# Kernel tuning notes

Measured on AMD Instinct MI355X. Metric: run time of the kernel, lower is better.

## Reference

```python
import jax, jax.numpy as jnp
import numpy as np

N_NODES = 100000
N_EDGES = 1600000
D_FEAT = 128
HIDDEN = 128
N_CLASSES = 10
NUM_GRAPHS = 64


def setup_inputs() -> dict:
    key = jax.random.key(0)
    ks = jax.random.split(key, 12)
    x = jax.random.normal(ks[0], (N_NODES, D_FEAT), dtype=jnp.float32)
    edge_index = jax.random.randint(ks[1], (2, N_EDGES), 0, N_NODES, dtype=jnp.int32)
    batch = jnp.sort(jax.random.randint(ks[2], (N_NODES,), 0, NUM_GRAPHS, dtype=jnp.int32))
    s = 1.0 / np.sqrt(HIDDEN)
    def lin(k, out_d, in_d):
        return jax.random.uniform(k, (out_d, in_d), jnp.float32, -s, s)
    return {
        "x": x,
        "edge_index": edge_index,
        "batch": batch,
        "W1l": lin(ks[3], HIDDEN, D_FEAT), "b1": jnp.zeros((HIDDEN,), jnp.float32),
        "W1r": lin(ks[4], HIDDEN, D_FEAT),
        "W2l": lin(ks[5], HIDDEN, HIDDEN), "b2": jnp.zeros((HIDDEN,), jnp.float32),
        "W2r": lin(ks[6], HIDDEN, HIDDEN),
        "W3l": lin(ks[7], HIDDEN, HIDDEN), "b3": jnp.zeros((HIDDEN,), jnp.float32),
        "W3r": lin(ks[8], HIDDEN, HIDDEN),
        "Wout": lin(ks[9], N_CLASSES, HIDDEN), "bout": jnp.zeros((N_CLASSES,), jnp.float32),
    }


def reference(x, edge_index, batch, W1l, b1, W1r, W2l, b2, W2r, W3l, b3, W3r, Wout, bout):
    src, dst = edge_index[0], edge_index[1]
    n = x.shape[0]

    def sage(h, Wl, b, Wr):
        # sum-aggregate neighbor features: scatter-add x[src] into dst rows
        agg = jax.ops.segment_sum(h[src], dst, num_segments=n)  # [N, d]
        return agg @ Wl.T + b + h @ Wr.T

    h = jax.nn.relu(sage(x, W1l, b1, W1r))
    h = jax.nn.relu(sage(h, W2l, b2, W2r))
    h = sage(h, W3l, b3, W3r)
    pooled = jax.ops.segment_sum(h, batch, num_segments=NUM_GRAPHS)  # [G, hidden]
    # dropout is identity in eval mode
    return pooled @ Wout.T + bout
```

## Files before the change

### kernel.cpp

```cpp
#include <hip/hip_runtime.h>
#include <hip/hip_bf16.h>

#define N_NODES  100000
#define N_EDGES  1600000
#define D_FEAT   128
#define HIDDEN   128
#define N_CLASSES 10
#define NUM_GRAPHS 64

#define NBUCK 250
#define NPB   400
#define BCAP  7168
#define GT    64
#define NPAD  100096
#define NTILES (NPAD / GT)

typedef __bf16 bf16x8 __attribute__((ext_vector_type(8)));
typedef float  f32x4  __attribute__((ext_vector_type(4)));

static __device__ __forceinline__ unsigned short f2bf(float f) {
    __bf16 b = (__bf16)f;
    return __builtin_bit_cast(unsigned short, b);
}

static __device__ __forceinline__ void async_copy16(void* lds, const void* g) {
    __builtin_amdgcn_global_load_lds(
        (const __attribute__((address_space(1))) void*)g,
        (__attribute__((address_space(3))) void*)lds, 16, 0, 0);
}

__global__ void conv_w6_kernel(const float* __restrict__ W0, const float* __restrict__ W1,
                               const float* __restrict__ W2, const float* __restrict__ W3,
                               const float* __restrict__ W4, const float* __restrict__ W5,
                               __bf16* __restrict__ out) {
    const float* Ws[6] = {W0, W1, W2, W3, W4, W5};
    int m = blockIdx.x >> 6;
    int i = (blockIdx.x & 63) * 256 + threadIdx.x;
    out[m * (HIDDEN * D_FEAT) + i] = (__bf16)Ws[m][i];
}

__global__ __launch_bounds__(256) void xconv_kernel(const float* __restrict__ x,
                                                    __bf16* __restrict__ out) {
    int i = blockIdx.x * 256 + threadIdx.x;
    bf16x8 o;
    if (i < N_NODES * 128 / 8) {
        float4 v0 = ((const float4*)x)[i * 2];
        float4 v1 = ((const float4*)x)[i * 2 + 1];
        o[0] = (__bf16)v0.x; o[1] = (__bf16)v0.y; o[2] = (__bf16)v0.z; o[3] = (__bf16)v0.w;
        o[4] = (__bf16)v1.x; o[5] = (__bf16)v1.y; o[6] = (__bf16)v1.z; o[7] = (__bf16)v1.w;
    } else {
        #pragma unroll
        for (int k = 0; k < 8; k++) o[k] = (__bf16)0.f;
    }
    if (i < NPAD * 128 / 8) ((bf16x8*)out)[i] = o;
}

__global__ __launch_bounds__(256) void bucket_scatter_kernel(const int* __restrict__ ei,
                                                             int* __restrict__ gcur,
                                                             int2* __restrict__ bkt) {
    __shared__ int h[NBUCK];
    __shared__ int lb[NBUCK];
    int t = threadIdx.x;
    const int CH = N_EDGES / 256;
    for (int i = t; i < NBUCK; i += 256) h[i] = 0;
    __syncthreads();
    int e0 = blockIdx.x * CH;
    for (int e = e0 + t; e < e0 + CH; e += 256) {
        int d = ei[N_EDGES + e];
        atomicAdd(&h[d / NPB], 1);
    }
    __syncthreads();
    for (int i = t; i < NBUCK; i += 256) {
        lb[i] = atomicAdd(&gcur[i], h[i]);
        h[i] = 0;
    }
    __syncthreads();
    for (int e = e0 + t; e < e0 + CH; e += 256) {
        int s = ei[e];
        int d = ei[N_EDGES + e];
        int bb = d / NPB;
        int pos = lb[bb] + atomicAdd(&h[bb], 1);
        if (pos < BCAP) bkt[(size_t)bb * BCAP + pos] = make_int2(s, d);
    }
}

__global__ __launch_bounds__(256) void bucket_csr_kernel(const int2* __restrict__ bkt,
                                                         const int* __restrict__ gcur,
                                                         int2* __restrict__ rpse,
                                                         int* __restrict__ csr_src) {
    const int b = blockIdx.x;
    const int n0 = b * NPB;
    const int base = b * BCAP;
    int m = gcur[b]; if (m > BCAP) m = BCAP;
    __shared__ int cnt[NPB];
    __shared__ int part[128];
    __shared__ int excl[NPB];
    int t = threadIdx.x;
    for (int i = t; i < NPB; i += 256) cnt[i] = 0;
    __syncthreads();
    for (int e = t; e < m; e += 256) {
        int2 p = bkt[base + e];
        atomicAdd(&cnt[p.y - n0], 1);
    }
    __syncthreads();
    int gs = 0;
    if (t < 100) { gs = cnt[4 * t] + cnt[4 * t + 1] + cnt[4 * t + 2] + cnt[4 * t + 3]; part[t] = gs; }
    else if (t < 128) part[t] = 0;
    __syncthreads();
    for (int off = 1; off < 128; off <<= 1) {
        int x = 0;
        if (t < 128 && t >= off) x = part[t - off];
        __syncthreads();
        if (t < 128) part[t] += x;
        __syncthreads();
    }
    if (t < 100) part[t] -= gs;
    __syncthreads();
    for (int i = t; i < NPB; i += 256) {
        int g = i >> 2;
        int e0 = part[g];
        for (int j = g * 4; j < i; j++) e0 += cnt[j];
        excl[i] = e0;
    }
    __syncthreads();
    for (int i = t; i < NPB; i += 256) {
        rpse[n0 + i] = make_int2(base + excl[i], base + excl[i] + cnt[i]);
    }
    __syncthreads();
    for (int i = t; i < NPB; i += 256) cnt[i] = excl[i];
    __syncthreads();
    for (int e = t; e < m; e += 256) {
        int2 p = bkt[base + e];
        int pos = base + atomicAdd(&cnt[p.y - n0], 1);
        csr_src[pos] = p.x;
    }
}

__global__ __launch_bounds__(256) void gather_kernel(
    const __bf16* __restrict__ h, const int2* __restrict__ rpse,
    const int* __restrict__ csr_src, __bf16* __restrict__ agg, int N)
{
    int nid = blockIdx.x * 16 + (threadIdx.x >> 4);
    if (nid >= N) return;
    int f8 = threadIdx.x & 15;
    int2 se = rpse[nid];

    float a[8] = {0.f, 0.f, 0.f, 0.f, 0.f, 0.f, 0.f, 0.f};

    int j = se.x;
    for (; j + 3 < se.y; j += 4) {
        int s0 = csr_src[j];
        int s1 = csr_src[j + 1];
        int s2 = csr_src[j + 2];
        int s3 = csr_src[j + 3];
        bf16x8 u0 = ((const bf16x8*)h)[(size_t)s0 * 16 + f8];
        bf16x8 u1 = ((const bf16x8*)h)[(size_t)s1 * 16 + f8];
        bf16x8 u2 = ((const bf16x8*)h)[(size_t)s2 * 16 + f8];
        bf16x8 u3 = ((const bf16x8*)h)[(size_t)s3 * 16 + f8];
        #pragma unroll
        for (int i = 0; i < 8; i++)
            a[i] += ((float)u0[i] + (float)u1[i]) + ((float)u2[i] + (float)u3[i]);
    }
    for (; j < se.y; j++) {
        int s0 = csr_src[j];
        bf16x8 u0 = ((const bf16x8*)h)[(size_t)s0 * 16 + f8];
        #pragma unroll
        for (int i = 0; i < 8; i++) a[i] += (float)u0[i];
    }
    bf16x8 o;
    #pragma unroll
    for (int i = 0; i < 8; i++) o[i] = (__bf16)a[i];
    ((bf16x8*)agg)[(size_t)nid * 16 + f8] = o;
}

template<bool RELU>
__global__ __launch_bounds__(256) void fused_gemm_kernel(
    const __bf16* __restrict__ hA,
    const __bf16* __restrict__ hG,
    const __bf16* __restrict__ Wl, const __bf16* __restrict__ Wr,
    const float* __restrict__ bias,
    __bf16* __restrict__ outp, int M)
{
    __shared__ __bf16 lds[2][GT * 128];

    const int tid  = threadIdx.x;
    const int wave = tid >> 6;
    const int lane = tid & 63;
    const int kq = lane >> 4;
    const int ln = lane & 15;
    const int node_base = blockIdx.x * GT;
    const int f_base = wave * 32;

    {
        const __bf16* gsrc = hG + (size_t)node_base * 128;
        const __bf16* asrc = hA + (size_t)node_base * 128;
        #pragma unroll
        for (int i = 0; i < 4; i++) {
            int u = i * 256 + tid;
            int row = u >> 4;
            int sc = (u & 15) ^ (row & 15);
            async_copy16(&lds[0][u * 8], gsrc + row * 128 + sc * 8);
            async_copy16(&lds[1][u * 8], asrc + row * 128 + sc * 8);
        }
    }

    bf16x8 wfragL[2][4], wfragR[2][4];
    #pragma unroll
    for (int t = 0; t < 2; t++) {
        int wrow = f_base + t * 16 + ln;
        #pragma unroll
        for (int kc = 0; kc < 4; kc++) {
            int k0 = kc * 32 + kq * 8;
            wfragL[t][kc] = *(const bf16x8*)(Wl + wrow * 128 + k0);
            wfragR[t][kc] = *(const bf16x8*)(Wr + wrow * 128 + k0);
        }
    }
    float4 bias4[2];
    bias4[0] = *(const float4*)(bias + f_base + kq * 4);
    bias4[1] = *(const float4*)(bias + f_base + 16 + kq * 4);

    __syncthreads();

    #pragma unroll 2
    for (int tau = 0; tau < GT / 16; tau++) {
        int r = tau * 16 + ln;
        bf16x8 gfrag[4], afrag[4];
        #pragma unroll
        for (int kc = 0; kc < 4; kc++) {
            int c = (4 * kc + kq) ^ ln;
            gfrag[kc] = *(const bf16x8*)&lds[0][r * 128 + c * 8];
            afrag[kc] = *(const bf16x8*)&lds[1][r * 128 + c * 8];
        }

        f32x4 acc[2] = {(f32x4)(0.f), (f32x4)(0.f)};
        #pragma unroll
        for (int kc = 0; kc < 4; kc++) {
            #pragma unroll
            for (int t = 0; t < 2; t++) {
                acc[t] = __builtin_amdgcn_mfma_f32_16x16x32_bf16(wfragL[t][kc], gfrag[kc], acc[t], 0, 0, 0);
                acc[t] = __builtin_amdgcn_mfma_f32_16x16x32_bf16(wfragR[t][kc], afrag[kc], acc[t], 0, 0, 0);
            }
        }

        int node = node_base + tau * 16 + ln;
        if (node < M) {
            size_t rowoff = (size_t)node * 128;
            #pragma unroll
            for (int t = 0; t < 2; t++) {
                int fc = f_base + t * 16 + kq * 4;
                ushort4 o;
                float v0 = acc[t][0] + bias4[t].x;
                float v1 = acc[t][1] + bias4[t].y;
                float v2 = acc[t][2] + bias4[t].z;
                float v3 = acc[t][3] + bias4[t].w;
                if (RELU) {
                    v0 = fmaxf(v0, 0.f); v1 = fmaxf(v1, 0.f);
                    v2 = fmaxf(v2, 0.f); v3 = fmaxf(v3, 0.f);
                }
                o.x = f2bf(v0); o.y = f2bf(v1); o.z = f2bf(v2); o.w = f2bf(v3);
                *(ushort4*)(outp + rowoff + fc) = o;
            }
        }
    }
}

__global__ __launch_bounds__(256) void pool_kernel(
    const __bf16* __restrict__ h, const int* __restrict__ batch,
    float* __restrict__ pooled, int N)
{
    int idx = blockIdx.x * 256 + threadIdx.x;
    int f = idx & 127;
    int chunk = idx >> 7;
    int n0 = chunk * 32;
    if (n0 >= N) return;
    int n1 = n0 + 32; if (n1 > N) n1 = N;
    int curb = batch[n0];
    float acc = 0.f;
    for (int n = n0; n < n1; n++) {
        int b = batch[n];
        if (b != curb) {
            unsafeAtomicAdd(&pooled[(size_t)curb * 128 + f], acc);
            acc = 0.f; curb = b;
        }
        acc += (float)h[(size_t)n * 128 + f];
    }
    unsafeAtomicAdd(&pooled[(size_t)curb * 128 + f], acc);
}

__global__ void final_gemm_kernel(
    const float* __restrict__ pooled, const float* __restrict__ Wout,
    const float* __restrict__ bout, float* __restrict__ out)
{
    int idx = blockIdx.x * 64 + threadIdx.x;
    if (idx < NUM_GRAPHS * N_CLASSES) {
        int g = idx / N_CLASSES;
        int c = idx % N_CLASSES;
        float acc = bout[c];
        for (int k = 0; k < HIDDEN; k++)
            acc += pooled[g * HIDDEN + k] * Wout[c * HIDDEN + k];
        out[idx] = acc;
    }
}

extern "C" void kernel_launch(void* const* d_in, const int* in_sizes, int n_in,
                              void* d_out, int out_size, void* d_ws, size_t ws_size,
                              hipStream_t stream) {
    const float* x     = (const float*)d_in[0];
    const int*   ei    = (const int*)d_in[1];
    const int*   batch = (const int*)d_in[2];
    const float* W1l = (const float*)d_in[3];
    const float* b1  = (const float*)d_in[4];
    const float* W1r = (const float*)d_in[5];
    const float* W2l = (const float*)d_in[6];
    const float* b2  = (const float*)d_in[7];
    const float* W2r = (const float*)d_in[8];
    const float* W3l = (const float*)d_in[9];
    const float* b3  = (const float*)d_in[10];
    const float* W3r = (const float*)d_in[11];
    const float* Wout = (const float*)d_in[12];
    const float* bout = (const float*)d_in[13];
    float* out = (float*)d_out;

    char* ws = (char*)d_ws;
    size_t off = 0;
    const size_t NB = (size_t)NPAD * 128 * sizeof(__bf16);
    __bf16* B0    = (__bf16*)(ws + off); off += NB;
    __bf16* B1    = (__bf16*)(ws + off); off += NB;
    __bf16* B2    = (__bf16*)(ws + off); off += NB;
    float* pooled = (float*)(ws + off);  off += (size_t)NUM_GRAPHS * HIDDEN * sizeof(float);
    __bf16* wbf   = (__bf16*)(ws + off); off += 6 * (size_t)HIDDEN * D_FEAT * sizeof(__bf16);
    int2* rpse    = (int2*)(ws + off);   off += (size_t)N_NODES * sizeof(int2);
    int* csr_src  = (int*)(ws + off);    off += (size_t)NBUCK * BCAP * sizeof(int);
    int2* bkt     = (int2*)(ws + off);   off += (size_t)NBUCK * BCAP * sizeof(int2);
    int* gcur     = (int*)(ws + off);    off += (NBUCK + 8) * sizeof(int);

    const int WSZ = HIDDEN * D_FEAT;

    conv_w6_kernel<<<6 * 64, 256, 0, stream>>>(W1l, W1r, W2l, W2r, W3l, W3r, wbf);
    xconv_kernel<<<NPAD * 128 / (256 * 8), 256, 0, stream>>>(x, B0);

    hipMemsetAsync(gcur, 0, NBUCK * sizeof(int), stream);
    bucket_scatter_kernel<<<256, 256, 0, stream>>>(ei, gcur, bkt);
    bucket_csr_kernel<<<NBUCK, 256, 0, stream>>>(bkt, gcur, rpse, csr_src);

    const int gath_grid = (N_NODES + 15) / 16;

    gather_kernel<<<gath_grid, 256, 0, stream>>>(B0, rpse, csr_src, B1, N_NODES);
    fused_gemm_kernel<true><<<NTILES, 256, 0, stream>>>(B0, B1, wbf + 0 * WSZ, wbf + 1 * WSZ, b1, B2, N_NODES);

    gather_kernel<<<gath_grid, 256, 0, stream>>>(B2, rpse, csr_src, B1, N_NODES);
    fused_gemm_kernel<true><<<NTILES, 256, 0, stream>>>(B2, B1, wbf + 2 * WSZ, wbf + 3 * WSZ, b2, B0, N_NODES);

    gather_kernel<<<gath_grid, 256, 0, stream>>>(B0, rpse, csr_src, B1, N_NODES);
    fused_gemm_kernel<false><<<NTILES, 256, 0, stream>>>(B0, B1, wbf + 4 * WSZ, wbf + 5 * WSZ, b3, B2, N_NODES);

    hipMemsetAsync(pooled, 0, (size_t)NUM_GRAPHS * HIDDEN * sizeof(float), stream);
    const int pool_grid = ((N_NODES + 31) / 32 * 128 + 255) / 256;
    pool_kernel<<<pool_grid, 256, 0, stream>>>(B2, batch, pooled, N_NODES);
    final_gemm_kernel<<<10, 64, 0, stream>>>(pooled, Wout, bout, out);
}
```

Before: 433.5 us.

## Fuse neighbor gather, dual GEMM, and pooling into one per-layer kernel

Merges the gather kernel and the fused GEMM into a single per-layer kernel. Each 16-node block aggregates neighbor features into LDS and then runs MFMA on them, so the intermediate aggregate buffer never goes to global memory. The last layer pools directly through shuffle-reduced atomics instead of writing h and running a separate pool kernel. Bucket entries are also packed into one 32-bit int instead of an int2, which halves the sort traffic. In exchange, the tiles are small, so every block reloads all weight fragments, and the final layer issues many more atomics.

```diff
diff --git a/kernel.cpp b/kernel.cpp
--- a/kernel.cpp
+++ b/kernel.cpp
@@ -11,9 +11,8 @@
 #define NBUCK 250
 #define NPB   400
 #define BCAP  7168
-#define GT    64
-#define NPAD  100096
-#define NTILES (NPAD / GT)
+#define TN    16
+#define NBLK  (N_NODES / TN)
 
 typedef __bf16 bf16x8 __attribute__((ext_vector_type(8)));
 typedef float  f32x4  __attribute__((ext_vector_type(4)));
@@ -21,12 +20,6 @@
 static __device__ __forceinline__ unsigned short f2bf(float f) {
     __bf16 b = (__bf16)f;
     return __builtin_bit_cast(unsigned short, b);
-}
-
-static __device__ __forceinline__ void async_copy16(void* lds, const void* g) {
-    __builtin_amdgcn_global_load_lds(
-        (const __attribute__((address_space(1))) void*)g,
-        (__attribute__((address_space(3))) void*)lds, 16, 0, 0);
 }
 
 __global__ void conv_w6_kernel(const float* __restrict__ W0, const float* __restrict__ W1,
@@ -42,22 +35,17 @@
 __global__ __launch_bounds__(256) void xconv_kernel(const float* __restrict__ x,
                                                     __bf16* __restrict__ out) {
     int i = blockIdx.x * 256 + threadIdx.x;
+    float4 v0 = ((const float4*)x)[i * 2];
+    float4 v1 = ((const float4*)x)[i * 2 + 1];
     bf16x8 o;
-    if (i < N_NODES * 128 / 8) {
-        float4 v0 = ((const float4*)x)[i * 2];
-        float4 v1 = ((const float4*)x)[i * 2 + 1];
-        o[0] = (__bf16)v0.x; o[1] = (__bf16)v0.y; o[2] = (__bf16)v0.z; o[3] = (__bf16)v0.w;
-        o[4] = (__bf16)v1.x; o[5] = (__bf16)v1.y; o[6] = (__bf16)v1.z; o[7] = (__bf16)v1.w;
-    } else {
-        #pragma unroll
-        for (int k = 0; k < 8; k++) o[k] = (__bf16)0.f;
-    }
-    if (i < NPAD * 128 / 8) ((bf16x8*)out)[i] = o;
+    o[0] = (__bf16)v0.x; o[1] = (__bf16)v0.y; o[2] = (__bf16)v0.z; o[3] = (__bf16)v0.w;
+    o[4] = (__bf16)v1.x; o[5] = (__bf16)v1.y; o[6] = (__bf16)v1.z; o[7] = (__bf16)v1.w;
+    ((bf16x8*)out)[i] = o;
 }
 
 __global__ __launch_bounds__(256) void bucket_scatter_kernel(const int* __restrict__ ei,
                                                              int* __restrict__ gcur,
-                                                             int2* __restrict__ bkt) {
+                                                             int* __restrict__ bkt) {
     __shared__ int h[NBUCK];
     __shared__ int lb[NBUCK];
     int t = threadIdx.x;
@@ -80,11 +68,11 @@
         int d = ei[N_EDGES + e];
         int bb = d / NPB;
         int pos = lb[bb] + atomicAdd(&h[bb], 1);
-        if (pos < BCAP) bkt[(size_t)bb * BCAP + pos] = make_int2(s, d);
-    }
-}
-
-__global__ __launch_bounds__(256) void bucket_csr_kernel(const int2* __restrict__ bkt,
+        if (pos < BCAP) bkt[(size_t)bb * BCAP + pos] = ((d - bb * NPB) << 17) | s;
+    }
+}
+
+__global__ __launch_bounds__(256) void bucket_csr_kernel(const int* __restrict__ bkt,
                                                          const int* __restrict__ gcur,
                                                          int2* __restrict__ rpse,
                                                          int* __restrict__ csr_src) {
@@ -99,8 +87,8 @@
     for (int i = t; i < NPB; i += 256) cnt[i] = 0;
     __syncthreads();
     for (int e = t; e < m; e += 256) {
-        int2 p = bkt[base + e];
-        atomicAdd(&cnt[p.y - n0], 1);
+        int p = bkt[base + e];
+        atomicAdd(&cnt[p >> 17], 1);
     }
     __syncthreads();
     int gs = 0;
@@ -130,79 +118,65 @@
     for (int i = t; i < NPB; i += 256) cnt[i] = excl[i];
     __syncthreads();
     for (int e = t; e < m; e += 256) {
-        int2 p = bkt[base + e];
-        int pos = base + atomicAdd(&cnt[p.y - n0], 1);
-        csr_src[pos] = p.x;
-    }
-}
-
-__global__ __launch_bounds__(256) void gather_kernel(
-    const __bf16* __restrict__ h, const int2* __restrict__ rpse,
-    const int* __restrict__ csr_src, __bf16* __restrict__ agg, int N)
-{
-    int nid = blockIdx.x * 16 + (threadIdx.x >> 4);
-    if (nid >= N) return;
-    int f8 = threadIdx.x & 15;
-    int2 se = rpse[nid];
-
-    float a[8] = {0.f, 0.f, 0.f, 0.f, 0.f, 0.f, 0.f, 0.f};
-
-    int j = se.x;
-    for (; j + 3 < se.y; j += 4) {
-        int s0 = csr_src[j];
-        int s1 = csr_src[j + 1];
-        int s2 = csr_src[j + 2];
-        int s3 = csr_src[j + 3];
-        bf16x8 u0 = ((const bf16x8*)h)[(size_t)s0 * 16 + f8];
-        bf16x8 u1 = ((const bf16x8*)h)[(size_t)s1 * 16 + f8];
-        bf16x8 u2 = ((const bf16x8*)h)[(size_t)s2 * 16 + f8];
-        bf16x8 u3 = ((const bf16x8*)h)[(size_t)s3 * 16 + f8];
-        #pragma unroll
-        for (int i = 0; i < 8; i++)
-            a[i] += ((float)u0[i] + (float)u1[i]) + ((float)u2[i] + (float)u3[i]);
-    }
-    for (; j < se.y; j++) {
-        int s0 = csr_src[j];
-        bf16x8 u0 = ((const bf16x8*)h)[(size_t)s0 * 16 + f8];
-        #pragma unroll
-        for (int i = 0; i < 8; i++) a[i] += (float)u0[i];
-    }
-    bf16x8 o;
-    #pragma unroll
-    for (int i = 0; i < 8; i++) o[i] = (__bf16)a[i];
-    ((bf16x8*)agg)[(size_t)nid * 16 + f8] = o;
-}
-
-template<bool RELU>
-__global__ __launch_bounds__(256) void fused_gemm_kernel(
-    const __bf16* __restrict__ hA,
-    const __bf16* __restrict__ hG,
+        int p = bkt[base + e];
+        int pos = base + atomicAdd(&cnt[p >> 17], 1);
+        csr_src[pos] = p & 0x1FFFF;
+    }
+}
+
+template<bool RELU, bool POOL>
+__global__ __launch_bounds__(256, 3) void fused_layer_kernel(
+    const __bf16* __restrict__ h,
+    const int2* __restrict__ rpse,
+    const int* __restrict__ csr_src,
     const __bf16* __restrict__ Wl, const __bf16* __restrict__ Wr,
     const float* __restrict__ bias,
-    __bf16* __restrict__ outp, int M)
+    __bf16* __restrict__ outp,
+    const int* __restrict__ batch,
+    float* __restrict__ pooled)
 {
-    __shared__ __bf16 lds[2][GT * 128];
-
-    const int tid  = threadIdx.x;
+    __shared__ __bf16 ldsT[TN * 128];
+
+    const int tid = threadIdx.x;
+    const int grp = tid >> 4;
+    const int f8  = tid & 15;
+    const int nid_base = blockIdx.x * TN;
+
+    {
+        const int node_g = nid_base + grp;
+        int2 se = rpse[node_g];
+        float a[8] = {0.f, 0.f, 0.f, 0.f, 0.f, 0.f, 0.f, 0.f};
+        int j = se.x;
+        for (; j + 3 < se.y; j += 4) {
+            int s0 = csr_src[j];
+            int s1 = csr_src[j + 1];
+            int s2 = csr_src[j + 2];
+            int s3 = csr_src[j + 3];
+            bf16x8 u0 = ((const bf16x8*)h)[(size_t)s0 * 16 + f8];
+            bf16x8 u1 = ((const bf16x8*)h)[(size_t)s1 * 16 + f8];
+            bf16x8 u2 = ((const bf16x8*)h)[(size_t)s2 * 16 + f8];
+            bf16x8 u3 = ((const bf16x8*)h)[(size_t)s3 * 16 + f8];
+            #pragma unroll
+            for (int i = 0; i < 8; i++)
+                a[i] += ((float)u0[i] + (float)u1[i]) + ((float)u2[i] + (float)u3[i]);
+        }
+        for (; j < se.y; j++) {
+            int s0 = csr_src[j];
+            bf16x8 u0 = ((const bf16x8*)h)[(size_t)s0 * 16 + f8];
+            #pragma unroll
+            for (int i = 0; i < 8; i++) a[i] += (float)u0[i];
+        }
+        bf16x8 o;
+        #pragma unroll
+        for (int i = 0; i < 8; i++) o[i] = (__bf16)a[i];
+        ((bf16x8*)ldsT)[grp * 16 + (f8 ^ grp)] = o;
+    }
+
     const int wave = tid >> 6;
     const int lane = tid & 63;
     const int kq = lane >> 4;
     const int ln = lane & 15;
-    const int node_base = blockIdx.x * GT;
     const int f_base = wave * 32;
-
-    {
-        const __bf16* gsrc = hG + (size_t)node_base * 128;
-        const __bf16* asrc = hA + (size_t)node_base * 128;
-        #pragma unroll
-        for (int i = 0; i < 4; i++) {
-            int u = i * 256 + tid;
-            int row = u >> 4;
-            int sc = (u & 15) ^ (row & 15);
-            async_copy16(&lds[0][u * 8], gsrc + row * 128 + sc * 8);
-            async_copy16(&lds[1][u * 8], asrc + row * 128 + sc * 8);
-        }
-    }
 
     bf16x8 wfragL[2][4], wfragR[2][4];
     #pragma unroll
@@ -219,72 +193,84 @@
     bias4[0] = *(const float4*)(bias + f_base + kq * 4);
     bias4[1] = *(const float4*)(bias + f_base + 16 + kq * 4);
 
-    __syncthreads();
-
-    #pragma unroll 2
-    for (int tau = 0; tau < GT / 16; tau++) {
-        int r = tau * 16 + ln;
-        bf16x8 gfrag[4], afrag[4];
-        #pragma unroll
-        for (int kc = 0; kc < 4; kc++) {
-            int c = (4 * kc + kq) ^ ln;
-            gfrag[kc] = *(const bf16x8*)&lds[0][r * 128 + c * 8];
-            afrag[kc] = *(const bf16x8*)&lds[1][r * 128 + c * 8];
-        }
-
-        f32x4 acc[2] = {(f32x4)(0.f), (f32x4)(0.f)};
-        #pragma unroll
-        for (int kc = 0; kc < 4; kc++) {
-            #pragma unroll
-            for (int t = 0; t < 2; t++) {
-                acc[t] = __builtin_amdgcn_mfma_f32_16x16x32_bf16(wfragL[t][kc], gfrag[kc], acc[t], 0, 0, 0);
-                acc[t] = __builtin_amdgcn_mfma_f32_16x16x32_bf16(wfragR[t][kc], afrag[kc], acc[t], 0, 0, 0);
+    const int node_s = nid_base + ln;
+    bf16x8 afrag[4];
+    #pragma unroll
+    for (int kc = 0; kc < 4; kc++)
+        afrag[kc] = *(const bf16x8*)(h + (size_t)node_s * 128 + kc * 32 + kq * 8);
+
+    __syncthreads();
+
+    bf16x8 gfrag[4];
+    #pragma unroll
+    for (int kc = 0; kc < 4; kc++)
+        gfrag[kc] = ((const bf16x8*)ldsT)[ln * 16 + ((4 * kc + kq) ^ ln)];
+
+    f32x4 acc[2] = {(f32x4)(0.f), (f32x4)(0.f)};
+    #pragma unroll
+    for (int kc = 0; kc < 4; kc++) {
+        #pragma unroll
+        for (int t = 0; t < 2; t++) {
+            acc[t] = __builtin_amdgcn_mfma_f32_16x16x32_bf16(wfragL[t][kc], gfrag[kc], acc[t], 0, 0, 0);
+            acc[t] = __builtin_amdgcn_mfma_f32_16x16x32_bf16(wfragR[t][kc], afrag[kc], acc[t], 0, 0, 0);
+        }
+    }
+
+    if (!POOL) {
+        size_t rowoff = (size_t)node_s * 128;
+        #pragma unroll
+        for (int t = 0; t < 2; t++) {
+            int fc = f_base + t * 16 + kq * 4;
+            float v0 = acc[t][0] + bias4[t].x;
+            float v1 = acc[t][1] + bias4[t].y;
+            float v2 = acc[t][2] + bias4[t].z;
+            float v3 = acc[t][3] + bias4[t].w;
+            if (RELU) {
+                v0 = fmaxf(v0, 0.f); v1 = fmaxf(v1, 0.f);
+                v2 = fmaxf(v2, 0.f); v3 = fmaxf(v3, 0.f);
             }
-        }
-
-        int node = node_base + tau * 16 + ln;
-        if (node < M) {
-            size_t rowoff = (size_t)node * 128;
-            #pragma unroll
-            for (int t = 0; t < 2; t++) {
-                int fc = f_base + t * 16 + kq * 4;
-                ushort4 o;
-                float v0 = acc[t][0] + bias4[t].x;
-                float v1 = acc[t][1] + bias4[t].y;
-                float v2 = acc[t][2] + bias4[t].z;
-                float v3 = acc[t][3] + bias4[t].w;
-                if (RELU) {
-                    v0 = fmaxf(v0, 0.f); v1 = fmaxf(v1, 0.f);
-                    v2 = fmaxf(v2, 0.f); v3 = fmaxf(v3, 0.f);
+            ushort4 o;
+            o.x = f2bf(v0); o.y = f2bf(v1); o.z = f2bf(v2); o.w = f2bf(v3);
+            *(ushort4*)(outp + rowoff + fc) = o;
+        }
+    } else {
+        const int b = batch[node_s];
+        const bool uni = (batch[nid_base] == batch[nid_base + TN - 1]);
+        #pragma unroll
+        for (int t = 0; t < 2; t++) {
+            int fc = f_base + t * 16 + kq * 4;
+            float v0 = acc[t][0] + bias4[t].x;
+            float v1 = acc[t][1] + bias4[t].y;
+            float v2 = acc[t][2] + bias4[t].z;
+            float v3 = acc[t][3] + bias4[t].w;
+            if (RELU) {
+                v0 = fmaxf(v0, 0.f); v1 = fmaxf(v1, 0.f);
+                v2 = fmaxf(v2, 0.f); v3 = fmaxf(v3, 0.f);
+            }
+            if (uni) {
+                #pragma unroll
+                for (int m = 1; m < 16; m <<= 1) {
+                    v0 += __shfl_xor(v0, m);
+                    v1 += __shfl_xor(v1, m);
+                    v2 += __shfl_xor(v2, m);
+                    v3 += __shfl_xor(v3, m);
                 }
-                o.x = f2bf(v0); o.y = f2bf(v1); o.z = f2bf(v2); o.w = f2bf(v3);
-                *(ushort4*)(outp + rowoff + fc) = o;
+                if (ln == 0) {
+                    float* p = &pooled[(size_t)b * HIDDEN + fc];
+                    unsafeAtomicAdd(p + 0, v0);
+                    unsafeAtomicAdd(p + 1, v1);
+                    unsafeAtomicAdd(p + 2, v2);
+                    unsafeAtomicAdd(p + 3, v3);
+                }
+            } else {
+                float* p = &pooled[(size_t)b * HIDDEN + fc];
+                unsafeAtomicAdd(p + 0, v0);
+                unsafeAtomicAdd(p + 1, v1);
+                unsafeAtomicAdd(p + 2, v2);
+                unsafeAtomicAdd(p + 3, v3);
             }
         }
     }
-}
-
-__global__ __launch_bounds__(256) void pool_kernel(
-    const __bf16* __restrict__ h, const int* __restrict__ batch,
-    float* __restrict__ pooled, int N)
-{
-    int idx = blockIdx.x * 256 + threadIdx.x;
-    int f = idx & 127;
-    int chunk = idx >> 7;
-    int n0 = chunk * 32;
-    if (n0 >= N) return;
-    int n1 = n0 + 32; if (n1 > N) n1 = N;
-    int curb = batch[n0];
-    float acc = 0.f;
-    for (int n = n0; n < n1; n++) {
-        int b = batch[n];
-        if (b != curb) {
-            unsafeAtomicAdd(&pooled[(size_t)curb * 128 + f], acc);
-            acc = 0.f; curb = b;
-        }
-        acc += (float)h[(size_t)n * 128 + f];
-    }
-    unsafeAtomicAdd(&pooled[(size_t)curb * 128 + f], acc);
 }
 
 __global__ void final_gemm_kernel(
@@ -323,39 +309,32 @@
 
     char* ws = (char*)d_ws;
     size_t off = 0;
-    const size_t NB = (size_t)NPAD * 128 * sizeof(__bf16);
+    const size_t NB = (size_t)N_NODES * 128 * sizeof(__bf16);
     __bf16* B0    = (__bf16*)(ws + off); off += NB;
-    __bf16* B1    = (__bf16*)(ws + off); off += NB;
     __bf16* B2    = (__bf16*)(ws + off); off += NB;
     float* pooled = (float*)(ws + off);  off += (size_t)NUM_GRAPHS * HIDDEN * sizeof(float);
     __bf16* wbf   = (__bf16*)(ws + off); off += 6 * (size_t)HIDDEN * D_FEAT * sizeof(__bf16);
     int2* rpse    = (int2*)(ws + off);   off += (size_t)N_NODES * sizeof(int2);
     int* csr_src  = (int*)(ws + off);    off += (size_t)NBUCK * BCAP * sizeof(int);
-    int2* bkt     = (int2*)(ws + off);   off += (size_t)NBUCK * BCAP * sizeof(int2);
+    int* bkt      = (int*)(ws + off);    off += (size_t)NBUCK * BCAP * sizeof(int);
     int* gcur     = (int*)(ws + off);    off += (NBUCK + 8) * sizeof(int);
 
     const int WSZ = HIDDEN * D_FEAT;
 
     conv_w6_kernel<<<6 * 64, 256, 0, stream>>>(W1l, W1r, W2l, W2r, W3l, W3r, wbf);
-    xconv_kernel<<<NPAD * 128 / (256 * 8), 256, 0, stream>>>(x, B0);
+    xconv_kernel<<<N_NODES * 128 / (256 * 8), 256, 0, stream>>>(x, B0);
 
     hipMemsetAsync(gcur, 0, NBUCK * sizeof(int), stream);
+    hipMemsetAsync(pooled, 0, (size_t)NUM_GRAPHS * HIDDEN * sizeof(float), stream);
     bucket_scatter_kernel<<<256, 256, 0, stream>>>(ei, gcur, bkt);
     bucket_csr_kernel<<<NBUCK, 256, 0, stream>>>(bkt, gcur, rpse, csr_src);
 
-    const int gath_grid = (N_NODES + 15) / 16;
-
-    gather_kernel<<<gath_grid, 256, 0, stream>>>(B0, rpse, csr_src, B1, N_NODES);
-    fused_gemm_kernel<true><<<NTILES, 256, 0, stream>>>(B0, B1, wbf + 0 * WSZ, wbf + 1 * WSZ, b1, B2, N_NODES);
-
-    gather_kernel<<<gath_grid, 256, 0, stream>>>(B2, rpse, csr_src, B1, N_NODES);
-    fused_gemm_kernel<true><<<NTILES, 256, 0, stream>>>(B2, B1, wbf + 2 * WSZ, wbf + 3 * WSZ, b2, B0, N_NODES);
-
-    gather_kernel<<<gath_grid, 256, 0, stream>>>(B0, rpse, csr_src, B1, N_NODES);
-    fused_gemm_kernel<false><<<NTILES, 256, 0, stream>>>(B0, B1, wbf + 4 * WSZ, wbf + 5 * WSZ, b3, B2, N_NODES);
-
-    hipMemsetAsync(pooled, 0, (size_t)NUM_GRAPHS * HIDDEN * sizeof(float), stream);
-    const int pool_grid = ((N_NODES + 31) / 32 * 128 + 255) / 256;
-    pool_kernel<<<pool_grid, 256, 0, stream>>>(B2, batch, pooled, N_NODES);
+    fused_layer_kernel<true, false><<<NBLK, 256, 0, stream>>>(
+        B0, rpse, csr_src, wbf + 0 * WSZ, wbf + 1 * WSZ, b1, B2, nullptr, nullptr);
+    fused_layer_kernel<true, false><<<NBLK, 256, 0, stream>>>(
+        B2, rpse, csr_src, wbf + 2 * WSZ, wbf + 3 * WSZ, b2, B0, nullptr, nullptr);
+    fused_layer_kernel<false, true><<<NBLK, 256, 0, stream>>>(
+        B0, rpse, csr_src, wbf + 4 * WSZ, wbf + 5 * WSZ, b3, nullptr, batch, pooled);
+
     final_gemm_kernel<<<10, 64, 0, stream>>>(pooled, Wout, bout, out);
 }
```

After: 565.2 us. 30.4% more time.
